# Kernel optimization log

Measured on AMD Instinct MI355X. Metric: run time of the kernel, lower is better.

The kernel has to match this reference:

```python
import jax, jax.numpy as jnp
import numpy as np

DIM = 512
HEADS = 8


def setup_inputs() -> dict:
    key = jax.random.key(0)
    ks = jax.random.split(key, 8)
    B, N_mm, N_a, N_v = 2, 64, 256, 256
    xmm = jax.random.normal(ks[0], (B, N_mm, DIM), dtype=jnp.float32)
    xa = jax.random.normal(ks[1], (B, N_a, DIM), dtype=jnp.float32)
    xv = jax.random.normal(ks[2], (B, N_v, DIM), dtype=jnp.float32)
    # Learned params (torch nn.Linear stores weight as [out, in]); qkv_bias=False, proj has bias.
    Wq = jax.random.normal(ks[3], (DIM, DIM), dtype=jnp.float32) * 0.02
    Wkv = jax.random.normal(ks[4], (2 * DIM, 2 * DIM), dtype=jnp.float32) * 0.02
    Wproj = jax.random.normal(ks[5], (DIM, DIM), dtype=jnp.float32) * 0.02
    bproj = jnp.zeros((DIM,), dtype=jnp.float32)
    return {"xmm": xmm, "xa": xa, "xv": xv, "Wq": Wq, "Wkv": Wkv, "Wproj": Wproj, "bproj": bproj}


def reference(xmm, xa, xv, Wq, Wkv, Wproj, bproj):
    B, N_mm, dim = xmm.shape
    N_v, N_a = xv.shape[1], xa.shape[1]
    H = HEADS
    hd = dim // H
    scale = hd ** (-0.5)

    # q: [B, H, N_mm, hd]
    q = (xmm @ Wq.T).reshape(B, N_mm, H, hd).transpose(0, 2, 1, 3)

    # kv(x_va) where x_va[b,i,j] = concat(xv[b,i], xa[b,j]); since kv is linear,
    # kv(x_va) = xv @ Wkv[:, :dim].T + xa @ Wkv[:, dim:].T, broadcast over the cartesian grid.
    pv = xv @ Wkv[:, :dim].T   # [B, N_v, 2*dim]
    pa = xa @ Wkv[:, dim:].T   # [B, N_a, 2*dim]
    kv = (pv[:, :, None, :] + pa[:, None, :, :]).reshape(B, N_v * N_a, 2, H, hd)
    k = kv[:, :, 0].transpose(0, 2, 1, 3)  # [B, H, N_v*N_a, hd]
    v = kv[:, :, 1].transpose(0, 2, 1, 3)  # [B, H, N_v*N_a, hd]

    attn = jax.nn.softmax(jnp.einsum('bhqd,bhkd->bhqk', q, k) * scale, axis=-1)
    out = jnp.einsum('bhqk,bhkd->bhqd', attn, v)          # [B, H, N_mm, hd]
    out = out.transpose(0, 2, 1, 3).reshape(B, N_mm, dim)  # [B, N_mm, dim]
    return out @ Wproj.T + bproj
```

## Files before the change

kernel.cpp:

```cpp
#include <hip/hip_runtime.h>


#define OQ16   0
#define OK16   65536
#define OVT16  589824
#define SIDESZ 262144
#define OHOUT16 1114112

typedef _Float16 f16x8 __attribute__((ext_vector_type(8)));
typedef _Float16 f16x4 __attribute__((ext_vector_type(4)));
typedef float f32x4 __attribute__((ext_vector_type(4)));

__device__ __forceinline__ void stage_tile_f16(
    const float* __restrict__ g, const float* __restrict__ g2, int ld,
    int base, int k0, _Float16* __restrict__ lds, int sr, int sq)
{
  const float* p = &g[(size_t)(base + sr) * ld + k0 + sq * 16];
  float4 v0 = *reinterpret_cast<const float4*>(p);
  float4 v1 = *reinterpret_cast<const float4*>(p + 4);
  float4 v2 = *reinterpret_cast<const float4*>(p + 8);
  float4 v3 = *reinterpret_cast<const float4*>(p + 12);
  if (g2) {
    const float* p2 = &g2[(size_t)(base + sr) * ld + k0 + sq * 16];
    float4 u0 = *reinterpret_cast<const float4*>(p2);
    float4 u1 = *reinterpret_cast<const float4*>(p2 + 4);
    float4 u2 = *reinterpret_cast<const float4*>(p2 + 8);
    float4 u3 = *reinterpret_cast<const float4*>(p2 + 12);
    v0.x += u0.x; v0.y += u0.y; v0.z += u0.z; v0.w += u0.w;
    v1.x += u1.x; v1.y += u1.y; v1.z += u1.z; v1.w += u1.w;
    v2.x += u2.x; v2.y += u2.y; v2.z += u2.z; v2.w += u2.w;
    v3.x += u3.x; v3.y += u3.y; v3.z += u3.z; v3.w += u3.w;
  }
  f16x8 h0 = {(_Float16)v0.x, (_Float16)v0.y, (_Float16)v0.z, (_Float16)v0.w,
              (_Float16)v1.x, (_Float16)v1.y, (_Float16)v1.z, (_Float16)v1.w};
  f16x8 h1 = {(_Float16)v2.x, (_Float16)v2.y, (_Float16)v2.z, (_Float16)v2.w,
              (_Float16)v3.x, (_Float16)v3.y, (_Float16)v3.z, (_Float16)v3.w};
  int c0 = (sq * 2) ^ (sr & 7);
  int c1 = (sq * 2 + 1) ^ (sr & 7);
  *reinterpret_cast<f16x8*>(&lds[sr * 64 + c0 * 8]) = h0;
  *reinterpret_cast<f16x8*>(&lds[sr * 64 + c1 * 8]) = h1;
}

template <int MODE>
__device__ __forceinline__ void mfma_gemm64(
    const float* __restrict__ A, const float* __restrict__ A2, int lda,
    const float* __restrict__ W, int ldw,
    int bm, int bn, int side,
    _Float16* __restrict__ ws16,
    float* __restrict__ Cf, int ldc, const float* __restrict__ bias)
{
  __shared__ _Float16 As[64 * 64];
  __shared__ _Float16 Ws[64 * 64];
  const int tid = threadIdx.x;
  const int lane = tid & 63;
  const int w = tid >> 6;
  const int wm = w >> 1, wn = w & 1;
  const int sr = tid >> 2;
  const int sq = tid & 3;

  f32x4 acc[2][2] = {};
  const int cl = lane & 15;
  const int kg = lane >> 4;

  for (int k0 = 0; k0 < 512; k0 += 64) {
    __syncthreads();
    stage_tile_f16(A, A2, lda, bm, k0, As, sr, sq);
    stage_tile_f16(W, nullptr, ldw, bn, k0, Ws, sr, sq);
    __syncthreads();
    #pragma unroll
    for (int ks = 0; ks < 2; ++ks) {
      f16x8 af[2], bf[2];
      #pragma unroll
      for (int mi = 0; mi < 2; ++mi) {
        int row = wm * 32 + mi * 16 + cl;
        int ch = (ks * 4 + kg) ^ (row & 7);
        af[mi] = *reinterpret_cast<const f16x8*>(&As[row * 64 + ch * 8]);
      }
      #pragma unroll
      for (int ni = 0; ni < 2; ++ni) {
        int col = wn * 32 + ni * 16 + cl;
        int ch = (ks * 4 + kg) ^ (col & 7);
        bf[ni] = *reinterpret_cast<const f16x8*>(&Ws[col * 64 + ch * 8]);
      }
      #pragma unroll
      for (int mi = 0; mi < 2; ++mi)
        #pragma unroll
        for (int ni = 0; ni < 2; ++ni)
          acc[mi][ni] = __builtin_amdgcn_mfma_f32_16x16x32_f16(
              af[mi], bf[ni], acc[mi][ni], 0, 0, 0);
    }
  }

  #pragma unroll
  for (int mi = 0; mi < 2; ++mi) {
    #pragma unroll
    for (int ni = 0; ni < 2; ++ni) {
      int row0 = bm + wm * 32 + mi * 16 + kg * 4;
      int col = bn + wn * 32 + ni * 16 + cl;
      if (MODE == 0) {
        int b = row0 >> 6, n = row0 & 63, h = col >> 6, d = col & 63;
        _Float16* dst = ws16 + OQ16 + (((size_t)b * 8 + h) * 64 + n) * 64 + d;
        #pragma unroll
        for (int r = 0; r < 4; ++r)
          dst[(size_t)r * 64] = (_Float16)(acc[mi][ni][r] * 0.125f);
      } else if (MODE == 1) {
        int b = row0 >> 8, key = row0 & 255;
        if (col < 512) {
          int h = col >> 6, d = col & 63;
          _Float16* dst = ws16 + OK16 + (size_t)side * SIDESZ +
                          (((size_t)b * 8 + h) * 256 + key) * 64 + d;
          #pragma unroll
          for (int r = 0; r < 4; ++r)
            dst[(size_t)r * 64] = (_Float16)acc[mi][ni][r];
        } else {
          int dp = col - 512;
          int h = dp >> 6, d = dp & 63;
          _Float16* dst = ws16 + OVT16 + (size_t)side * SIDESZ +
                          (((size_t)b * 8 + h) * 64 + d) * 256 + key;
          f16x4 v = {(_Float16)acc[mi][ni][0], (_Float16)acc[mi][ni][1],
                     (_Float16)acc[mi][ni][2], (_Float16)acc[mi][ni][3]};
          *reinterpret_cast<f16x4*>(dst) = v;
        }
      } else {
        float bv = bias ? bias[col] : 0.f;
        #pragma unroll
        for (int r = 0; r < 4; ++r)
          Cf[(size_t)(row0 + r) * ldc + col] = acc[mi][ni][r] + bv;
      }
    }
  }
}

__global__ __launch_bounds__(256) void fused_proj_kernel(
    const float* __restrict__ xmm, const float* __restrict__ xa,
    const float* __restrict__ xv, const float* __restrict__ Wq,
    const float* __restrict__ Wkv, _Float16* __restrict__ ws16)
{
  const int id = blockIdx.x;
  if (id < 16) {
    mfma_gemm64<0>(xmm, nullptr, 512, Wq, 512, (id >> 3) * 64, (id & 7) * 64,
                   0, ws16, nullptr, 0, nullptr);
  } else if (id < 144) {
    int t = id - 16;
    mfma_gemm64<1>(xv, nullptr, 512, Wkv, 1024, (t >> 4) * 64, (t & 15) * 64,
                   0, ws16, nullptr, 0, nullptr);
  } else {
    int t = id - 144;
    mfma_gemm64<1>(xa, nullptr, 512, Wkv + 512, 1024, (t >> 4) * 64,
                   (t & 15) * 64, 1, ws16, nullptr, 0, nullptr);
  }
}

__global__ __launch_bounds__(256) void proj_out_kernel(
    const _Float16* __restrict__ ws16, const float* __restrict__ Wproj,
    const float* __restrict__ bproj, float* __restrict__ out)
{
  const float* hv = (const float*)(ws16 + OHOUT16);
  const float* ha = hv + 65536;
  mfma_gemm64<2>(hv, ha, 512, Wproj, 512,
                 (int)(blockIdx.x >> 3) * 64, (int)(blockIdx.x & 7) * 64, 0,
                 nullptr, out, 512, bproj);
}

__global__ __launch_bounds__(512) void attn_kernel(
    const _Float16* __restrict__ ws16, float* __restrict__ hv,
    float* __restrict__ ha)
{
  __shared__ __align__(16) _Float16 smem[55552];
  _Float16* Kl = smem;
  _Float16* Vl = smem + 16384;
  _Float16* Ql = smem + 32768;
  _Float16* P  = smem + 36864;
  float* m_s  = (float*)(smem + 53248);
  float* l_s  = m_s + 512;
  float* Mtot = l_s + 512;
  float* Ltot = Mtot + 64;

  const int x = blockIdx.x;
  const int side = x & 1;
  const int bh = x >> 1;
  const int b = bh >> 3, h = bh & 7;

  const int tid = threadIdx.x;
  const int w = tid >> 6;
  const int lane = tid & 63;
  const int l15 = lane & 15;
  const int kg = lane >> 4;

  const _Float16* gQ = ws16 + OQ16 + (size_t)bh * 4096;
  const _Float16* gK = ws16 + OK16 + (size_t)side * SIDESZ + (size_t)bh * 16384;
  const _Float16* gV = ws16 + OVT16 + (size_t)side * SIDESZ + (size_t)bh * 16384;

  {
    int ch = tid;
    int row = ch >> 3, c = ch & 7;
    *reinterpret_cast<f16x8*>(&Ql[row * 64 + ((c ^ (row & 7)) * 8)]) =
        *reinterpret_cast<const f16x8*>(&gQ[ch * 8]);
  }
  #pragma unroll
  for (int i = 0; i < 4; ++i) {
    int ch = tid + i * 512;
    int row = ch >> 3, c = ch & 7;
    *reinterpret_cast<f16x8*>(&Kl[row * 64 + ((c ^ (row & 7)) * 8)]) =
        *reinterpret_cast<const f16x8*>(&gK[ch * 8]);
  }
  #pragma unroll
  for (int i = 0; i < 4; ++i) {
    int ch = tid + i * 512;
    int row = ch >> 5, c = ch & 31;
    *reinterpret_cast<f16x8*>(&Vl[row * 256 + ((c ^ (row & 7)) * 8)]) =
        *reinterpret_cast<const f16x8*>(&gV[ch * 8]);
  }
  __syncthreads();

  f16x8 qb[4][2];
  #pragma unroll
  for (int qf = 0; qf < 4; ++qf)
    #pragma unroll
    for (int ks = 0; ks < 2; ++ks)
      qb[qf][ks] = *reinterpret_cast<const f16x8*>(
          &Ql[(qf * 16 + l15) * 64 + (((ks * 4 + kg) ^ (l15 & 7)) * 8)]);

  f32x4 st[2][4] = {};
  #pragma unroll
  for (int kf = 0; kf < 2; ++kf) {
    int krow = w * 32 + kf * 16 + l15;
    #pragma unroll
    for (int ks = 0; ks < 2; ++ks) {
      f16x8 af = *reinterpret_cast<const f16x8*>(
          &Kl[krow * 64 + (((ks * 4 + kg) ^ (l15 & 7)) * 8)]);
      #pragma unroll
      for (int qf = 0; qf < 4; ++qf)
        st[kf][qf] = __builtin_amdgcn_mfma_f32_16x16x32_f16(
            af, qb[qf][ks], st[kf][qf], 0, 0, 0);
    }
  }

  float mx[4];
  #pragma unroll
  for (int qf = 0; qf < 4; ++qf) {
    float m = st[0][qf][0];
    #pragma unroll
    for (int kf = 0; kf < 2; ++kf)
      #pragma unroll
      for (int r = 0; r < 4; ++r) m = fmaxf(m, st[kf][qf][r]);
    m = fmaxf(m, __shfl_xor(m, 16));
    m = fmaxf(m, __shfl_xor(m, 32));
    mx[qf] = m;
  }
  if (kg == 0) {
    #pragma unroll
    for (int qf = 0; qf < 4; ++qf) m_s[w * 64 + qf * 16 + l15] = mx[qf];
  }
  __syncthreads();
  if (tid < 64) {
    float M = m_s[tid];
    #pragma unroll
    for (int w2 = 1; w2 < 8; ++w2) M = fmaxf(M, m_s[w2 * 64 + tid]);
    Mtot[tid] = M;
  }
  __syncthreads();

  #pragma unroll
  for (int qf = 0; qf < 4; ++qf) {
    float M = Mtot[qf * 16 + l15];
    float ls = 0.f;
    #pragma unroll
    for (int kf = 0; kf < 2; ++kf)
      #pragma unroll
      for (int r = 0; r < 4; ++r) {
        float e = __expf(st[kf][qf][r] - M);
        st[kf][qf][r] = e;
        ls += e;
      }
    ls += __shfl_xor(ls, 16);
    ls += __shfl_xor(ls, 32);
    if (kg == 0) l_s[w * 64 + qf * 16 + l15] = ls;
    #pragma unroll
    for (int kf = 0; kf < 2; ++kf) {
      int q = qf * 16 + l15;
      int chunk = w * 4 + kf * 2 + (kg >> 1);
      f16x4 pk = {(_Float16)st[kf][qf][0], (_Float16)st[kf][qf][1],
                  (_Float16)st[kf][qf][2], (_Float16)st[kf][qf][3]};
      *reinterpret_cast<f16x4*>(
          &P[q * 256 + ((chunk ^ (q & 7)) * 8) + (kg & 1) * 4]) = pk;
    }
  }
  __syncthreads();
  if (tid < 64) {
    float L = l_s[tid];
    #pragma unroll
    for (int w2 = 1; w2 < 8; ++w2) L += l_s[w2 * 64 + tid];
    Ltot[tid] = L;
  }
  __syncthreads();

  const int qf = w & 3;
  const int d0 = (w >> 2) * 2;
  f32x4 oc[2] = {};
  #pragma unroll
  for (int ks = 0; ks < 8; ++ks) {
    f16x8 pa = *reinterpret_cast<const f16x8*>(
        &P[(qf * 16 + l15) * 256 + (((ks * 4 + kg) ^ (l15 & 7)) * 8)]);
    #pragma unroll
    for (int j = 0; j < 2; ++j) {
      int d = (d0 + j) * 16 + l15;
      f16x8 vb = *reinterpret_cast<const f16x8*>(
          &Vl[d * 256 + (((ks * 4 + kg) ^ (d & 7)) * 8)]);
      oc[j] = __builtin_amdgcn_mfma_f32_16x16x32_f16(pa, vb, oc[j], 0, 0, 0);
    }
  }

  float* houtS = side ? ha : hv;
  #pragma unroll
  for (int j = 0; j < 2; ++j)
    #pragma unroll
    for (int r = 0; r < 4; ++r) {
      int q = qf * 16 + kg * 4 + r;
      int d = (d0 + j) * 16 + l15;
      houtS[(size_t)(b * 64 + q) * 512 + h * 64 + d] =
          oc[j][r] * (1.0f / Ltot[q]);
    }
}

extern "C" void kernel_launch(void* const* d_in, const int* in_sizes, int n_in,
                              void* d_out, int out_size, void* d_ws, size_t ws_size,
                              hipStream_t stream) {
  const float* xmm   = (const float*)d_in[0];
  const float* xa    = (const float*)d_in[1];
  const float* xv    = (const float*)d_in[2];
  const float* Wq    = (const float*)d_in[3];
  const float* Wkv   = (const float*)d_in[4];
  const float* Wproj = (const float*)d_in[5];
  const float* bproj = (const float*)d_in[6];
  float* out = (float*)d_out;
  _Float16* ws16 = (_Float16*)d_ws;
  float* hv = (float*)(ws16 + OHOUT16);
  float* ha = hv + 65536;

  fused_proj_kernel<<<272, 256, 0, stream>>>(xmm, xa, xv, Wq, Wkv, ws16);
  attn_kernel<<<32, 512, 0, stream>>>(ws16, hv, ha);
  proj_out_kernel<<<16, 256, 0, stream>>>(ws16, Wproj, bproj, out);
}
```

Measured before the change: 34.56 us.

## Fuse projection, attention and output GEMM into one persistent kernel with grid barriers

The three kernel launches are merged into a single 256-block kernel that separates the QKV projection, attention and output projection stages with atomic-counter grid barriers. The 272 projection tiles are spread over 256 blocks, with the last 16 blocks each doing two tiles. Attention is reshaped to 256 threads per block, and the GEMM mainloop now prefetches the next K-slice into registers while the current one is computed. This removes launch gaps between stages but adds a memset launch, spin-wait barriers that rely on all blocks being co-resident, and fewer threads per attention block.

Measured after the change: 81.72 us. 2.36x slower.

```diff
diff --git a/kernel.cpp b/kernel.cpp
--- a/kernel.cpp
+++ b/kernel.cpp
@@ -6,35 +6,53 @@
 #define OVT16  589824
 #define SIDESZ 262144
 #define OHOUT16 1114112
+#define BAR_BYTE_OFF (4u << 20)
+#define NBLK 256
 
 typedef _Float16 f16x8 __attribute__((ext_vector_type(8)));
 typedef _Float16 f16x4 __attribute__((ext_vector_type(4)));
 typedef float f32x4 __attribute__((ext_vector_type(4)));
 
-__device__ __forceinline__ void stage_tile_f16(
+__device__ __forceinline__ void gbar(int* cnt)
+{
+  __syncthreads();
+  if (threadIdx.x == 0) {
+    __threadfence();
+    __hip_atomic_fetch_add(cnt, 1, __ATOMIC_RELAXED, __HIP_MEMORY_SCOPE_AGENT);
+    while (__hip_atomic_load(cnt, __ATOMIC_RELAXED,
+                             __HIP_MEMORY_SCOPE_AGENT) < NBLK)
+      __builtin_amdgcn_s_sleep(2);
+    __threadfence();
+  }
+  __syncthreads();
+}
+
+__device__ __forceinline__ void load_regs(
     const float* __restrict__ g, const float* __restrict__ g2, int ld,
-    int base, int k0, _Float16* __restrict__ lds, int sr, int sq)
+    int base, int k0, int sr, int sq, float4* r)
 {
   const float* p = &g[(size_t)(base + sr) * ld + k0 + sq * 16];
-  float4 v0 = *reinterpret_cast<const float4*>(p);
-  float4 v1 = *reinterpret_cast<const float4*>(p + 4);
-  float4 v2 = *reinterpret_cast<const float4*>(p + 8);
-  float4 v3 = *reinterpret_cast<const float4*>(p + 12);
+  r[0] = *reinterpret_cast<const float4*>(p);
+  r[1] = *reinterpret_cast<const float4*>(p + 4);
+  r[2] = *reinterpret_cast<const float4*>(p + 8);
+  r[3] = *reinterpret_cast<const float4*>(p + 12);
   if (g2) {
     const float* p2 = &g2[(size_t)(base + sr) * ld + k0 + sq * 16];
-    float4 u0 = *reinterpret_cast<const float4*>(p2);
-    float4 u1 = *reinterpret_cast<const float4*>(p2 + 4);
-    float4 u2 = *reinterpret_cast<const float4*>(p2 + 8);
-    float4 u3 = *reinterpret_cast<const float4*>(p2 + 12);
-    v0.x += u0.x; v0.y += u0.y; v0.z += u0.z; v0.w += u0.w;
-    v1.x += u1.x; v1.y += u1.y; v1.z += u1.z; v1.w += u1.w;
-    v2.x += u2.x; v2.y += u2.y; v2.z += u2.z; v2.w += u2.w;
-    v3.x += u3.x; v3.y += u3.y; v3.z += u3.z; v3.w += u3.w;
-  }
-  f16x8 h0 = {(_Float16)v0.x, (_Float16)v0.y, (_Float16)v0.z, (_Float16)v0.w,
-              (_Float16)v1.x, (_Float16)v1.y, (_Float16)v1.z, (_Float16)v1.w};
-  f16x8 h1 = {(_Float16)v2.x, (_Float16)v2.y, (_Float16)v2.z, (_Float16)v2.w,
-              (_Float16)v3.x, (_Float16)v3.y, (_Float16)v3.z, (_Float16)v3.w};
+    #pragma unroll
+    for (int i = 0; i < 4; ++i) {
+      float4 u = *reinterpret_cast<const float4*>(p2 + 4 * i);
+      r[i].x += u.x; r[i].y += u.y; r[i].z += u.z; r[i].w += u.w;
+    }
+  }
+}
+
+__device__ __forceinline__ void store_lds(
+    _Float16* __restrict__ lds, int sr, int sq, const float4* r)
+{
+  f16x8 h0 = {(_Float16)r[0].x, (_Float16)r[0].y, (_Float16)r[0].z, (_Float16)r[0].w,
+              (_Float16)r[1].x, (_Float16)r[1].y, (_Float16)r[1].z, (_Float16)r[1].w};
+  f16x8 h1 = {(_Float16)r[2].x, (_Float16)r[2].y, (_Float16)r[2].z, (_Float16)r[2].w,
+              (_Float16)r[3].x, (_Float16)r[3].y, (_Float16)r[3].z, (_Float16)r[3].w};
   int c0 = (sq * 2) ^ (sr & 7);
   int c1 = (sq * 2 + 1) ^ (sr & 7);
   *reinterpret_cast<f16x8*>(&lds[sr * 64 + c0 * 8]) = h0;
@@ -42,15 +60,14 @@
 }
 
 template <int MODE>
-__device__ __forceinline__ void mfma_gemm64(
+__device__ void gemm_task(
     const float* __restrict__ A, const float* __restrict__ A2, int lda,
     const float* __restrict__ W, int ldw,
     int bm, int bn, int side,
     _Float16* __restrict__ ws16,
-    float* __restrict__ Cf, int ldc, const float* __restrict__ bias)
-{
-  __shared__ _Float16 As[64 * 64];
-  __shared__ _Float16 Ws[64 * 64];
+    float* __restrict__ Cf, int ldc, const float* __restrict__ bias,
+    _Float16* __restrict__ As, _Float16* __restrict__ Ws)
+{
   const int tid = threadIdx.x;
   const int lane = tid & 63;
   const int w = tid >> 6;
@@ -62,10 +79,19 @@
   const int cl = lane & 15;
   const int kg = lane >> 4;
 
-  for (int k0 = 0; k0 < 512; k0 += 64) {
+  float4 ra[2][4], rw[2][4];
+  load_regs(A, A2, lda, bm, 0, sr, sq, ra[0]);
+  load_regs(W, nullptr, ldw, bn, 0, sr, sq, rw[0]);
+
+  #pragma unroll
+  for (int s = 0; s < 8; ++s) {
     __syncthreads();
-    stage_tile_f16(A, A2, lda, bm, k0, As, sr, sq);
-    stage_tile_f16(W, nullptr, ldw, bn, k0, Ws, sr, sq);
+    store_lds(As, sr, sq, ra[s & 1]);
+    store_lds(Ws, sr, sq, rw[s & 1]);
+    if (s < 7) {
+      load_regs(A, A2, lda, bm, (s + 1) * 64, sr, sq, ra[(s + 1) & 1]);
+      load_regs(W, nullptr, ldw, bn, (s + 1) * 64, sr, sq, rw[(s + 1) & 1]);
+    }
     __syncthreads();
     #pragma unroll
     for (int ks = 0; ks < 2; ++ks) {
@@ -131,52 +157,19 @@
   }
 }
 
-__global__ __launch_bounds__(256) void fused_proj_kernel(
-    const float* __restrict__ xmm, const float* __restrict__ xa,
-    const float* __restrict__ xv, const float* __restrict__ Wq,
-    const float* __restrict__ Wkv, _Float16* __restrict__ ws16)
-{
-  const int id = blockIdx.x;
-  if (id < 16) {
-    mfma_gemm64<0>(xmm, nullptr, 512, Wq, 512, (id >> 3) * 64, (id & 7) * 64,
-                   0, ws16, nullptr, 0, nullptr);
-  } else if (id < 144) {
-    int t = id - 16;
-    mfma_gemm64<1>(xv, nullptr, 512, Wkv, 1024, (t >> 4) * 64, (t & 15) * 64,
-                   0, ws16, nullptr, 0, nullptr);
-  } else {
-    int t = id - 144;
-    mfma_gemm64<1>(xa, nullptr, 512, Wkv + 512, 1024, (t >> 4) * 64,
-                   (t & 15) * 64, 1, ws16, nullptr, 0, nullptr);
-  }
-}
-
-__global__ __launch_bounds__(256) void proj_out_kernel(
-    const _Float16* __restrict__ ws16, const float* __restrict__ Wproj,
-    const float* __restrict__ bproj, float* __restrict__ out)
-{
-  const float* hv = (const float*)(ws16 + OHOUT16);
-  const float* ha = hv + 65536;
-  mfma_gemm64<2>(hv, ha, 512, Wproj, 512,
-                 (int)(blockIdx.x >> 3) * 64, (int)(blockIdx.x & 7) * 64, 0,
-                 nullptr, out, 512, bproj);
-}
-
-__global__ __launch_bounds__(512) void attn_kernel(
+__device__ void attn_task(
     const _Float16* __restrict__ ws16, float* __restrict__ hv,
-    float* __restrict__ ha)
-{
-  __shared__ __align__(16) _Float16 smem[55552];
+    float* __restrict__ ha, int x, _Float16* __restrict__ smem)
+{
   _Float16* Kl = smem;
   _Float16* Vl = smem + 16384;
   _Float16* Ql = smem + 32768;
   _Float16* P  = smem + 36864;
   float* m_s  = (float*)(smem + 53248);
-  float* l_s  = m_s + 512;
-  float* Mtot = l_s + 512;
+  float* l_s  = m_s + 256;
+  float* Mtot = l_s + 256;
   float* Ltot = Mtot + 64;
 
-  const int x = blockIdx.x;
   const int side = x & 1;
   const int bh = x >> 1;
   const int b = bh >> 3, h = bh & 7;
@@ -191,22 +184,23 @@
   const _Float16* gK = ws16 + OK16 + (size_t)side * SIDESZ + (size_t)bh * 16384;
   const _Float16* gV = ws16 + OVT16 + (size_t)side * SIDESZ + (size_t)bh * 16384;
 
-  {
-    int ch = tid;
+  #pragma unroll
+  for (int i = 0; i < 2; ++i) {
+    int ch = tid + i * 256;
     int row = ch >> 3, c = ch & 7;
     *reinterpret_cast<f16x8*>(&Ql[row * 64 + ((c ^ (row & 7)) * 8)]) =
         *reinterpret_cast<const f16x8*>(&gQ[ch * 8]);
   }
   #pragma unroll
-  for (int i = 0; i < 4; ++i) {
-    int ch = tid + i * 512;
+  for (int i = 0; i < 8; ++i) {
+    int ch = tid + i * 256;
     int row = ch >> 3, c = ch & 7;
     *reinterpret_cast<f16x8*>(&Kl[row * 64 + ((c ^ (row & 7)) * 8)]) =
         *reinterpret_cast<const f16x8*>(&gK[ch * 8]);
   }
   #pragma unroll
-  for (int i = 0; i < 4; ++i) {
-    int ch = tid + i * 512;
+  for (int i = 0; i < 8; ++i) {
+    int ch = tid + i * 256;
     int row = ch >> 5, c = ch & 31;
     *reinterpret_cast<f16x8*>(&Vl[row * 256 + ((c ^ (row & 7)) * 8)]) =
         *reinterpret_cast<const f16x8*>(&gV[ch * 8]);
@@ -221,10 +215,10 @@
       qb[qf][ks] = *reinterpret_cast<const f16x8*>(
           &Ql[(qf * 16 + l15) * 64 + (((ks * 4 + kg) ^ (l15 & 7)) * 8)]);
 
-  f32x4 st[2][4] = {};
-  #pragma unroll
-  for (int kf = 0; kf < 2; ++kf) {
-    int krow = w * 32 + kf * 16 + l15;
+  f32x4 st[4][4] = {};
+  #pragma unroll
+  for (int kf = 0; kf < 4; ++kf) {
+    int krow = w * 64 + kf * 16 + l15;
     #pragma unroll
     for (int ks = 0; ks < 2; ++ks) {
       f16x8 af = *reinterpret_cast<const f16x8*>(
@@ -236,27 +230,21 @@
     }
   }
 
-  float mx[4];
   #pragma unroll
   for (int qf = 0; qf < 4; ++qf) {
     float m = st[0][qf][0];
     #pragma unroll
-    for (int kf = 0; kf < 2; ++kf)
+    for (int kf = 0; kf < 4; ++kf)
       #pragma unroll
       for (int r = 0; r < 4; ++r) m = fmaxf(m, st[kf][qf][r]);
     m = fmaxf(m, __shfl_xor(m, 16));
     m = fmaxf(m, __shfl_xor(m, 32));
-    mx[qf] = m;
-  }
-  if (kg == 0) {
-    #pragma unroll
-    for (int qf = 0; qf < 4; ++qf) m_s[w * 64 + qf * 16 + l15] = mx[qf];
+    if (kg == 0) m_s[w * 64 + qf * 16 + l15] = m;
   }
   __syncthreads();
   if (tid < 64) {
-    float M = m_s[tid];
-    #pragma unroll
-    for (int w2 = 1; w2 < 8; ++w2) M = fmaxf(M, m_s[w2 * 64 + tid]);
+    float M = fmaxf(fmaxf(m_s[tid], m_s[64 + tid]),
+                    fmaxf(m_s[128 + tid], m_s[192 + tid]));
     Mtot[tid] = M;
   }
   __syncthreads();
@@ -266,7 +254,7 @@
     float M = Mtot[qf * 16 + l15];
     float ls = 0.f;
     #pragma unroll
-    for (int kf = 0; kf < 2; ++kf)
+    for (int kf = 0; kf < 4; ++kf)
       #pragma unroll
       for (int r = 0; r < 4; ++r) {
         float e = __expf(st[kf][qf][r] - M);
@@ -277,9 +265,9 @@
     ls += __shfl_xor(ls, 32);
     if (kg == 0) l_s[w * 64 + qf * 16 + l15] = ls;
     #pragma unroll
-    for (int kf = 0; kf < 2; ++kf) {
+    for (int kf = 0; kf < 4; ++kf) {
       int q = qf * 16 + l15;
-      int chunk = w * 4 + kf * 2 + (kg >> 1);
+      int chunk = w * 8 + kf * 2 + (kg >> 1);
       f16x4 pk = {(_Float16)st[kf][qf][0], (_Float16)st[kf][qf][1],
                   (_Float16)st[kf][qf][2], (_Float16)st[kf][qf][3]};
       *reinterpret_cast<f16x4*>(
@@ -288,39 +276,80 @@
   }
   __syncthreads();
   if (tid < 64) {
-    float L = l_s[tid];
-    #pragma unroll
-    for (int w2 = 1; w2 < 8; ++w2) L += l_s[w2 * 64 + tid];
-    Ltot[tid] = L;
-  }
-  __syncthreads();
-
-  const int qf = w & 3;
-  const int d0 = (w >> 2) * 2;
-  f32x4 oc[2] = {};
+    Ltot[tid] = l_s[tid] + l_s[64 + tid] + l_s[128 + tid] + l_s[192 + tid];
+  }
+  __syncthreads();
+
+  f32x4 oc[4] = {};
   #pragma unroll
   for (int ks = 0; ks < 8; ++ks) {
     f16x8 pa = *reinterpret_cast<const f16x8*>(
-        &P[(qf * 16 + l15) * 256 + (((ks * 4 + kg) ^ (l15 & 7)) * 8)]);
-    #pragma unroll
-    for (int j = 0; j < 2; ++j) {
-      int d = (d0 + j) * 16 + l15;
+        &P[(w * 16 + l15) * 256 + (((ks * 4 + kg) ^ (l15 & 7)) * 8)]);
+    #pragma unroll
+    for (int nf = 0; nf < 4; ++nf) {
+      int d = nf * 16 + l15;
       f16x8 vb = *reinterpret_cast<const f16x8*>(
           &Vl[d * 256 + (((ks * 4 + kg) ^ (d & 7)) * 8)]);
-      oc[j] = __builtin_amdgcn_mfma_f32_16x16x32_f16(pa, vb, oc[j], 0, 0, 0);
+      oc[nf] = __builtin_amdgcn_mfma_f32_16x16x32_f16(pa, vb, oc[nf], 0, 0, 0);
     }
   }
 
   float* houtS = side ? ha : hv;
   #pragma unroll
-  for (int j = 0; j < 2; ++j)
+  for (int nf = 0; nf < 4; ++nf)
     #pragma unroll
     for (int r = 0; r < 4; ++r) {
-      int q = qf * 16 + kg * 4 + r;
-      int d = (d0 + j) * 16 + l15;
+      int q = w * 16 + kg * 4 + r;
+      int d = nf * 16 + l15;
       houtS[(size_t)(b * 64 + q) * 512 + h * 64 + d] =
-          oc[j][r] * (1.0f / Ltot[q]);
-    }
+          oc[nf][r] * (1.0f / Ltot[q]);
+    }
+}
+
+__global__ __launch_bounds__(256) void fused_all_kernel(
+    const float* __restrict__ xmm, const float* __restrict__ xa,
+    const float* __restrict__ xv, const float* __restrict__ Wq,
+    const float* __restrict__ Wkv, const float* __restrict__ Wproj,
+    const float* __restrict__ bproj, float* __restrict__ out,
+    _Float16* __restrict__ ws16, int* __restrict__ bar)
+{
+  __shared__ __align__(16) _Float16 smem[54528];
+  _Float16* As = smem;
+  _Float16* Ws = smem + 4096;
+  const int bid = blockIdx.x;
+
+  {
+    int t = bid;
+    if (t < 16) {
+      gemm_task<0>(xmm, nullptr, 512, Wq, 512, (t >> 3) * 64, (t & 7) * 64, 0,
+                   ws16, nullptr, 0, nullptr, As, Ws);
+    } else if (t < 144) {
+      int u = t - 16;
+      gemm_task<1>(xv, nullptr, 512, Wkv, 1024, (u >> 4) * 64, (u & 15) * 64,
+                   0, ws16, nullptr, 0, nullptr, As, Ws);
+    } else {
+      int u = t - 144;
+      gemm_task<1>(xa, nullptr, 512, Wkv + 512, 1024, (u >> 4) * 64,
+                   (u & 15) * 64, 1, ws16, nullptr, 0, nullptr, As, Ws);
+    }
+    if (bid >= 240) {
+      int u = bid - 240 + 112;
+      gemm_task<1>(xa, nullptr, 512, Wkv + 512, 1024, (u >> 4) * 64,
+                   (u & 15) * 64, 1, ws16, nullptr, 0, nullptr, As, Ws);
+    }
+  }
+  gbar(bar);
+
+  float* hv = (float*)(ws16 + OHOUT16);
+  float* ha = hv + 65536;
+  if (bid < 32) attn_task(ws16, hv, ha, bid, smem);
+  gbar(bar + 1);
+
+  if (bid >= 32 && bid < 48) {
+    int t = bid - 32;
+    gemm_task<2>(hv, ha, 512, Wproj, 512, (t >> 3) * 64, (t & 7) * 64, 0,
+                 nullptr, out, 512, bproj, As, Ws);
+  }
 }
 
 extern "C" void kernel_launch(void* const* d_in, const int* in_sizes, int n_in,
@@ -335,10 +364,9 @@
   const float* bproj = (const float*)d_in[6];
   float* out = (float*)d_out;
   _Float16* ws16 = (_Float16*)d_ws;
-  float* hv = (float*)(ws16 + OHOUT16);
-  float* ha = hv + 65536;
-
-  fused_proj_kernel<<<272, 256, 0, stream>>>(xmm, xa, xv, Wq, Wkv, ws16);
-  attn_kernel<<<32, 512, 0, stream>>>(ws16, hv, ha);
-  proj_out_kernel<<<16, 256, 0, stream>>>(ws16, Wproj, bproj, out);
-}
+  int* bar = (int*)((char*)d_ws + BAR_BYTE_OFF);
+
+  hipMemsetAsync(bar, 0, 8, stream);
+  fused_all_kernel<<<NBLK, 256, 0, stream>>>(
+      xmm, xa, xv, Wq, Wkv, Wproj, bproj, out, ws16, bar);
+}
```

## Fuse Q/K/V projections into per-(batch,head,side) attention kernel

Applied to the files above, without the earlier changes.

Removes the separate projection kernel and its fp16 workspace round trip. Each of the 32 attention blocks now computes its own head's Q, K and V projection slices with MFMA, reading fp32 inputs and weights directly from global memory without LDS staging, then writes them into the swizzled LDS layout the attention code already uses. This saves a kernel launch and the global write/read of K, V and Q. In exchange only 32 blocks do all the projection work, and the Q projection is computed twice because both sides compute it, which may underuse the GPU compared with the 272-block projection grid.

New measurement: 98.18 us. 2.84x slower.

```diff
diff --git a/kernel.cpp b/kernel.cpp
--- a/kernel.cpp
+++ b/kernel.cpp
@@ -1,169 +1,23 @@
 #include <hip/hip_runtime.h>
 
-
-#define OQ16   0
-#define OK16   65536
-#define OVT16  589824
-#define SIDESZ 262144
-#define OHOUT16 1114112
 
 typedef _Float16 f16x8 __attribute__((ext_vector_type(8)));
 typedef _Float16 f16x4 __attribute__((ext_vector_type(4)));
 typedef float f32x4 __attribute__((ext_vector_type(4)));
 
-__device__ __forceinline__ void stage_tile_f16(
-    const float* __restrict__ g, const float* __restrict__ g2, int ld,
-    int base, int k0, _Float16* __restrict__ lds, int sr, int sq)
+__device__ __forceinline__ f16x8 ld_cvt(const float* __restrict__ p)
 {
-  const float* p = &g[(size_t)(base + sr) * ld + k0 + sq * 16];
-  float4 v0 = *reinterpret_cast<const float4*>(p);
-  float4 v1 = *reinterpret_cast<const float4*>(p + 4);
-  float4 v2 = *reinterpret_cast<const float4*>(p + 8);
-  float4 v3 = *reinterpret_cast<const float4*>(p + 12);
-  if (g2) {
-    const float* p2 = &g2[(size_t)(base + sr) * ld + k0 + sq * 16];
-    float4 u0 = *reinterpret_cast<const float4*>(p2);
-    float4 u1 = *reinterpret_cast<const float4*>(p2 + 4);
-    float4 u2 = *reinterpret_cast<const float4*>(p2 + 8);
-    float4 u3 = *reinterpret_cast<const float4*>(p2 + 12);
-    v0.x += u0.x; v0.y += u0.y; v0.z += u0.z; v0.w += u0.w;
-    v1.x += u1.x; v1.y += u1.y; v1.z += u1.z; v1.w += u1.w;
-    v2.x += u2.x; v2.y += u2.y; v2.z += u2.z; v2.w += u2.w;
-    v3.x += u3.x; v3.y += u3.y; v3.z += u3.z; v3.w += u3.w;
-  }
-  f16x8 h0 = {(_Float16)v0.x, (_Float16)v0.y, (_Float16)v0.z, (_Float16)v0.w,
-              (_Float16)v1.x, (_Float16)v1.y, (_Float16)v1.z, (_Float16)v1.w};
-  f16x8 h1 = {(_Float16)v2.x, (_Float16)v2.y, (_Float16)v2.z, (_Float16)v2.w,
-              (_Float16)v3.x, (_Float16)v3.y, (_Float16)v3.z, (_Float16)v3.w};
-  int c0 = (sq * 2) ^ (sr & 7);
-  int c1 = (sq * 2 + 1) ^ (sr & 7);
-  *reinterpret_cast<f16x8*>(&lds[sr * 64 + c0 * 8]) = h0;
-  *reinterpret_cast<f16x8*>(&lds[sr * 64 + c1 * 8]) = h1;
-}
-
-template <int MODE>
-__device__ __forceinline__ void mfma_gemm64(
-    const float* __restrict__ A, const float* __restrict__ A2, int lda,
-    const float* __restrict__ W, int ldw,
-    int bm, int bn, int side,
-    _Float16* __restrict__ ws16,
-    float* __restrict__ Cf, int ldc, const float* __restrict__ bias)
-{
-  __shared__ _Float16 As[64 * 64];
-  __shared__ _Float16 Ws[64 * 64];
-  const int tid = threadIdx.x;
-  const int lane = tid & 63;
-  const int w = tid >> 6;
-  const int wm = w >> 1, wn = w & 1;
-  const int sr = tid >> 2;
-  const int sq = tid & 3;
-
-  f32x4 acc[2][2] = {};
-  const int cl = lane & 15;
-  const int kg = lane >> 4;
-
-  for (int k0 = 0; k0 < 512; k0 += 64) {
-    __syncthreads();
-    stage_tile_f16(A, A2, lda, bm, k0, As, sr, sq);
-    stage_tile_f16(W, nullptr, ldw, bn, k0, Ws, sr, sq);
-    __syncthreads();
-    #pragma unroll
-    for (int ks = 0; ks < 2; ++ks) {
-      f16x8 af[2], bf[2];
-      #pragma unroll
-      for (int mi = 0; mi < 2; ++mi) {
-        int row = wm * 32 + mi * 16 + cl;
-        int ch = (ks * 4 + kg) ^ (row & 7);
-        af[mi] = *reinterpret_cast<const f16x8*>(&As[row * 64 + ch * 8]);
-      }
-      #pragma unroll
-      for (int ni = 0; ni < 2; ++ni) {
-        int col = wn * 32 + ni * 16 + cl;
-        int ch = (ks * 4 + kg) ^ (col & 7);
-        bf[ni] = *reinterpret_cast<const f16x8*>(&Ws[col * 64 + ch * 8]);
-      }
-      #pragma unroll
-      for (int mi = 0; mi < 2; ++mi)
-        #pragma unroll
-        for (int ni = 0; ni < 2; ++ni)
-          acc[mi][ni] = __builtin_amdgcn_mfma_f32_16x16x32_f16(
-              af[mi], bf[ni], acc[mi][ni], 0, 0, 0);
-    }
-  }
-
-  #pragma unroll
-  for (int mi = 0; mi < 2; ++mi) {
-    #pragma unroll
-    for (int ni = 0; ni < 2; ++ni) {
-      int row0 = bm + wm * 32 + mi * 16 + kg * 4;
-      int col = bn + wn * 32 + ni * 16 + cl;
-      if (MODE == 0) {
-        int b = row0 >> 6, n = row0 & 63, h = col >> 6, d = col & 63;
-        _Float16* dst = ws16 + OQ16 + (((size_t)b * 8 + h) * 64 + n) * 64 + d;
-        #pragma unroll
-        for (int r = 0; r < 4; ++r)
-          dst[(size_t)r * 64] = (_Float16)(acc[mi][ni][r] * 0.125f);
-      } else if (MODE == 1) {
-        int b = row0 >> 8, key = row0 & 255;
-        if (col < 512) {
-          int h = col >> 6, d = col & 63;
-          _Float16* dst = ws16 + OK16 + (size_t)side * SIDESZ +
-                          (((size_t)b * 8 + h) * 256 + key) * 64 + d;
-          #pragma unroll
-          for (int r = 0; r < 4; ++r)
-            dst[(size_t)r * 64] = (_Float16)acc[mi][ni][r];
-        } else {
-          int dp = col - 512;
-          int h = dp >> 6, d = dp & 63;
-          _Float16* dst = ws16 + OVT16 + (size_t)side * SIDESZ +
-                          (((size_t)b * 8 + h) * 64 + d) * 256 + key;
-          f16x4 v = {(_Float16)acc[mi][ni][0], (_Float16)acc[mi][ni][1],
-                     (_Float16)acc[mi][ni][2], (_Float16)acc[mi][ni][3]};
-          *reinterpret_cast<f16x4*>(dst) = v;
-        }
-      } else {
-        float bv = bias ? bias[col] : 0.f;
-        #pragma unroll
-        for (int r = 0; r < 4; ++r)
-          Cf[(size_t)(row0 + r) * ldc + col] = acc[mi][ni][r] + bv;
-      }
-    }
-  }
-}
-
-__global__ __launch_bounds__(256) void fused_proj_kernel(
+  float4 u = *reinterpret_cast<const float4*>(p);
+  float4 v = *reinterpret_cast<const float4*>(p + 4);
+  f16x8 h = {(_Float16)u.x, (_Float16)u.y, (_Float16)u.z, (_Float16)u.w,
+             (_Float16)v.x, (_Float16)v.y, (_Float16)v.z, (_Float16)v.w};
+  return h;
+}
+
+__global__ __launch_bounds__(512) void fused_bh_kernel(
     const float* __restrict__ xmm, const float* __restrict__ xa,
     const float* __restrict__ xv, const float* __restrict__ Wq,
-    const float* __restrict__ Wkv, _Float16* __restrict__ ws16)
-{
-  const int id = blockIdx.x;
-  if (id < 16) {
-    mfma_gemm64<0>(xmm, nullptr, 512, Wq, 512, (id >> 3) * 64, (id & 7) * 64,
-                   0, ws16, nullptr, 0, nullptr);
-  } else if (id < 144) {
-    int t = id - 16;
-    mfma_gemm64<1>(xv, nullptr, 512, Wkv, 1024, (t >> 4) * 64, (t & 15) * 64,
-                   0, ws16, nullptr, 0, nullptr);
-  } else {
-    int t = id - 144;
-    mfma_gemm64<1>(xa, nullptr, 512, Wkv + 512, 1024, (t >> 4) * 64,
-                   (t & 15) * 64, 1, ws16, nullptr, 0, nullptr);
-  }
-}
-
-__global__ __launch_bounds__(256) void proj_out_kernel(
-    const _Float16* __restrict__ ws16, const float* __restrict__ Wproj,
-    const float* __restrict__ bproj, float* __restrict__ out)
-{
-  const float* hv = (const float*)(ws16 + OHOUT16);
-  const float* ha = hv + 65536;
-  mfma_gemm64<2>(hv, ha, 512, Wproj, 512,
-                 (int)(blockIdx.x >> 3) * 64, (int)(blockIdx.x & 7) * 64, 0,
-                 nullptr, out, 512, bproj);
-}
-
-__global__ __launch_bounds__(512) void attn_kernel(
-    const _Float16* __restrict__ ws16, float* __restrict__ hv,
+    const float* __restrict__ Wkv, float* __restrict__ hv,
     float* __restrict__ ha)
 {
   __shared__ __align__(16) _Float16 smem[55552];
@@ -176,10 +30,10 @@
   float* Mtot = l_s + 512;
   float* Ltot = Mtot + 64;
 
-  const int x = blockIdx.x;
-  const int side = x & 1;
-  const int bh = x >> 1;
-  const int b = bh >> 3, h = bh & 7;
+  const int bid = blockIdx.x;
+  const int side = bid & 1;
+  const int h = (bid >> 1) & 7;
+  const int b = bid >> 4;
 
   const int tid = threadIdx.x;
   const int w = tid >> 6;
@@ -187,29 +41,79 @@
   const int l15 = lane & 15;
   const int kg = lane >> 4;
 
-  const _Float16* gQ = ws16 + OQ16 + (size_t)bh * 4096;
-  const _Float16* gK = ws16 + OK16 + (size_t)side * SIDESZ + (size_t)bh * 16384;
-  const _Float16* gV = ws16 + OVT16 + (size_t)side * SIDESZ + (size_t)bh * 16384;
-
+  const float* X = (side ? xa : xv) + (size_t)b * 256 * 512;
+  const float* xmm_b = xmm + (size_t)b * 64 * 512;
+
+  const int kgrp = (w >> 1) * 4;
+  const int dgrp = (w & 1) * 2;
+  const int qf0 = w * 2;
+  const int nfq = qf0 >> 2;
+  const int dq0 = qf0 & 3, dq1 = (qf0 + 1) & 3;
+
+  f32x4 ak[4][2] = {};
+  f32x4 av[4][2] = {};
+  f32x4 aq[2] = {};
+
+  #pragma unroll 2
+  for (int kk = 0; kk < 16; ++kk) {
+    const int k0 = kk * 32 + kg * 8;
+    f16x8 xf[4], wk[2], wvv[2];
+    #pragma unroll
+    for (int i = 0; i < 4; ++i)
+      xf[i] = ld_cvt(&X[(size_t)((kgrp + i) * 16 + l15) * 512 + k0]);
+    #pragma unroll
+    for (int j = 0; j < 2; ++j) {
+      const int d = (dgrp + j) * 16 + l15;
+      wk[j]  = ld_cvt(&Wkv[(size_t)(h * 64 + d) * 1024 + side * 512 + k0]);
+      wvv[j] = ld_cvt(&Wkv[(size_t)(512 + h * 64 + d) * 1024 + side * 512 + k0]);
+    }
+    f16x8 xq  = ld_cvt(&xmm_b[(size_t)(nfq * 16 + l15) * 512 + k0]);
+    f16x8 wq0 = ld_cvt(&Wq[(size_t)(h * 64 + dq0 * 16 + l15) * 512 + k0]);
+    f16x8 wq1 = ld_cvt(&Wq[(size_t)(h * 64 + dq1 * 16 + l15) * 512 + k0]);
+
+    #pragma unroll
+    for (int i = 0; i < 4; ++i)
+      #pragma unroll
+      for (int j = 0; j < 2; ++j) {
+        ak[i][j] = __builtin_amdgcn_mfma_f32_16x16x32_f16(
+            xf[i], wk[j], ak[i][j], 0, 0, 0);
+        av[i][j] = __builtin_amdgcn_mfma_f32_16x16x32_f16(
+            xf[i], wvv[j], av[i][j], 0, 0, 0);
+      }
+    aq[0] = __builtin_amdgcn_mfma_f32_16x16x32_f16(xq, wq0, aq[0], 0, 0, 0);
+    aq[1] = __builtin_amdgcn_mfma_f32_16x16x32_f16(xq, wq1, aq[1], 0, 0, 0);
+  }
+
+  #pragma unroll
+  for (int i = 0; i < 4; ++i)
+    #pragma unroll
+    for (int j = 0; j < 2; ++j) {
+      const int d = (dgrp + j) * 16 + l15;
+      const int dch = d >> 3;
+      #pragma unroll
+      for (int r = 0; r < 4; ++r) {
+        const int key = (kgrp + i) * 16 + kg * 4 + r;
+        Kl[key * 64 + ((dch ^ (key & 7)) * 8) + (d & 7)] =
+            (_Float16)ak[i][j][r];
+      }
+      const int chv = (kgrp + i) * 2 + (kg >> 1);
+      f16x4 vv4 = {(_Float16)av[i][j][0], (_Float16)av[i][j][1],
+                   (_Float16)av[i][j][2], (_Float16)av[i][j][3]};
+      *reinterpret_cast<f16x4*>(
+          &Vl[d * 256 + ((chv ^ (d & 7)) * 8) + (kg & 1) * 4]) = vv4;
+    }
   {
-    int ch = tid;
-    int row = ch >> 3, c = ch & 7;
-    *reinterpret_cast<f16x8*>(&Ql[row * 64 + ((c ^ (row & 7)) * 8)]) =
-        *reinterpret_cast<const f16x8*>(&gQ[ch * 8]);
-  }
-  #pragma unroll
-  for (int i = 0; i < 4; ++i) {
-    int ch = tid + i * 512;
-    int row = ch >> 3, c = ch & 7;
-    *reinterpret_cast<f16x8*>(&Kl[row * 64 + ((c ^ (row & 7)) * 8)]) =
-        *reinterpret_cast<const f16x8*>(&gK[ch * 8]);
-  }
-  #pragma unroll
-  for (int i = 0; i < 4; ++i) {
-    int ch = tid + i * 512;
-    int row = ch >> 5, c = ch & 31;
-    *reinterpret_cast<f16x8*>(&Vl[row * 256 + ((c ^ (row & 7)) * 8)]) =
-        *reinterpret_cast<const f16x8*>(&gV[ch * 8]);
+    const int dqs[2] = {dq0 * 16 + l15, dq1 * 16 + l15};
+    #pragma unroll
+    for (int e = 0; e < 2; ++e) {
+      const int dq = dqs[e];
+      #pragma unroll
+      for (int r = 0; r < 4; ++r) {
+        const int n = nfq * 16 + kg * 4 + r;
+        Ql[n * 64 + (((dq >> 3) ^ (n & 7)) * 8) + (dq & 7)] =
+            (_Float16)(aq[e][r] * 0.125f);
+      }
+    }
   }
   __syncthreads();
 
@@ -320,6 +224,93 @@
       int d = (d0 + j) * 16 + l15;
       houtS[(size_t)(b * 64 + q) * 512 + h * 64 + d] =
           oc[j][r] * (1.0f / Ltot[q]);
+    }
+}
+
+__device__ __forceinline__ void stage_sum_f16(
+    const float* __restrict__ g, const float* __restrict__ g2, int ld,
+    int base, int k0, _Float16* __restrict__ lds, int sr, int sq)
+{
+  const float* p = &g[(size_t)(base + sr) * ld + k0 + sq * 16];
+  const float* p2 = g2 ? &g2[(size_t)(base + sr) * ld + k0 + sq * 16] : nullptr;
+  float4 v[4];
+  #pragma unroll
+  for (int i = 0; i < 4; ++i) {
+    v[i] = *reinterpret_cast<const float4*>(p + 4 * i);
+    if (p2) {
+      float4 u = *reinterpret_cast<const float4*>(p2 + 4 * i);
+      v[i].x += u.x; v[i].y += u.y; v[i].z += u.z; v[i].w += u.w;
+    }
+  }
+  f16x8 h0 = {(_Float16)v[0].x, (_Float16)v[0].y, (_Float16)v[0].z, (_Float16)v[0].w,
+              (_Float16)v[1].x, (_Float16)v[1].y, (_Float16)v[1].z, (_Float16)v[1].w};
+  f16x8 h1 = {(_Float16)v[2].x, (_Float16)v[2].y, (_Float16)v[2].z, (_Float16)v[2].w,
+              (_Float16)v[3].x, (_Float16)v[3].y, (_Float16)v[3].z, (_Float16)v[3].w};
+  int c0 = (sq * 2) ^ (sr & 7);
+  int c1 = (sq * 2 + 1) ^ (sr & 7);
+  *reinterpret_cast<f16x8*>(&lds[sr * 64 + c0 * 8]) = h0;
+  *reinterpret_cast<f16x8*>(&lds[sr * 64 + c1 * 8]) = h1;
+}
+
+__global__ __launch_bounds__(256) void proj_out_kernel(
+    const float* __restrict__ hv, const float* __restrict__ ha,
+    const float* __restrict__ Wproj, const float* __restrict__ bproj,
+    float* __restrict__ out)
+{
+  __shared__ _Float16 As[64 * 64];
+  __shared__ _Float16 Ws[64 * 64];
+  const int bm = (int)(blockIdx.x >> 3) * 64;
+  const int bn = (int)(blockIdx.x & 7) * 64;
+  const int tid = threadIdx.x;
+  const int lane = tid & 63;
+  const int w = tid >> 6;
+  const int wm = w >> 1, wn = w & 1;
+  const int sr = tid >> 2;
+  const int sq = tid & 3;
+
+  f32x4 acc[2][2] = {};
+  const int cl = lane & 15;
+  const int kg = lane >> 4;
+
+  for (int k0 = 0; k0 < 512; k0 += 64) {
+    __syncthreads();
+    stage_sum_f16(hv, ha, 512, bm, k0, As, sr, sq);
+    stage_sum_f16(Wproj, nullptr, 512, bn, k0, Ws, sr, sq);
+    __syncthreads();
+    #pragma unroll
+    for (int ks = 0; ks < 2; ++ks) {
+      f16x8 af[2], bf[2];
+      #pragma unroll
+      for (int mi = 0; mi < 2; ++mi) {
+        int row = wm * 32 + mi * 16 + cl;
+        int ch = (ks * 4 + kg) ^ (row & 7);
+        af[mi] = *reinterpret_cast<const f16x8*>(&As[row * 64 + ch * 8]);
+      }
+      #pragma unroll
+      for (int ni = 0; ni < 2; ++ni) {
+        int col = wn * 32 + ni * 16 + cl;
+        int ch = (ks * 4 + kg) ^ (col & 7);
+        bf[ni] = *reinterpret_cast<const f16x8*>(&Ws[col * 64 + ch * 8]);
+      }
+      #pragma unroll
+      for (int mi = 0; mi < 2; ++mi)
+        #pragma unroll
+        for (int ni = 0; ni < 2; ++ni)
+          acc[mi][ni] = __builtin_amdgcn_mfma_f32_16x16x32_f16(
+              af[mi], bf[ni], acc[mi][ni], 0, 0, 0);
+    }
+  }
+
+  #pragma unroll
+  for (int mi = 0; mi < 2; ++mi)
+    #pragma unroll
+    for (int ni = 0; ni < 2; ++ni) {
+      int row0 = bm + wm * 32 + mi * 16 + kg * 4;
+      int col = bn + wn * 32 + ni * 16 + cl;
+      float bv = bproj[col];
+      #pragma unroll
+      for (int r = 0; r < 4; ++r)
+        out[(size_t)(row0 + r) * 512 + col] = acc[mi][ni][r] + bv;
     }
 }
 
@@ -334,11 +325,9 @@
   const float* Wproj = (const float*)d_in[5];
   const float* bproj = (const float*)d_in[6];
   float* out = (float*)d_out;
-  _Float16* ws16 = (_Float16*)d_ws;
-  float* hv = (float*)(ws16 + OHOUT16);
+  float* hv = (float*)d_ws;
   float* ha = hv + 65536;
 
-  fused_proj_kernel<<<272, 256, 0, stream>>>(xmm, xa, xv, Wq, Wkv, ws16);
-  attn_kernel<<<32, 512, 0, stream>>>(ws16, hv, ha);
-  proj_out_kernel<<<16, 256, 0, stream>>>(ws16, Wproj, bproj, out);
-}
+  fused_bh_kernel<<<32, 512, 0, stream>>>(xmm, xa, xv, Wq, Wkv, hv, ha);
+  proj_out_kernel<<<16, 256, 0, stream>>>(hv, ha, Wproj, bproj, out);
+}
```
